# Optimization experiments

Hardware: AMD Instinct MI355X
Metric: run time of the kernel (lower is better)

Reference implementation:

```python
import jax, jax.numpy as jnp
import numpy as np
import math

INPUT_SIZE = 2048
HIDDEN_SIZE = 2048
BATCH = 4096


def setup_inputs() -> dict:
    key = jax.random.key(0)
    ks = jax.random.split(key, 16)
    stdv = 1.0 / math.sqrt(HIDDEN_SIZE)

    def u(k, shape):
        return jax.random.uniform(k, shape, jnp.float32, -stdv, stdv)

    inp = {
        "x": jax.random.normal(ks[0], (BATCH, INPUT_SIZE), jnp.float32),
        "h_x": jax.random.normal(ks[1], (BATCH, HIDDEN_SIZE), jnp.float32),
        "c_x": jax.random.normal(ks[2], (BATCH, HIDDEN_SIZE), jnp.float32),
        "W_xi": u(ks[3], (INPUT_SIZE, HIDDEN_SIZE)),
        "W_hi": u(ks[4], (HIDDEN_SIZE, HIDDEN_SIZE)),
        "b_i": u(ks[5], (HIDDEN_SIZE,)),
        "W_xf": u(ks[6], (INPUT_SIZE, HIDDEN_SIZE)),
        "W_hf": u(ks[7], (HIDDEN_SIZE, HIDDEN_SIZE)),
        "b_f": u(ks[8], (HIDDEN_SIZE,)),
        "W_xc": u(ks[9], (INPUT_SIZE, HIDDEN_SIZE)),
        "W_hc": u(ks[10], (HIDDEN_SIZE, HIDDEN_SIZE)),
        "b_c": u(ks[11], (HIDDEN_SIZE,)),
        "W_xo": u(ks[12], (INPUT_SIZE, HIDDEN_SIZE)),
        "W_ho": u(ks[13], (HIDDEN_SIZE, HIDDEN_SIZE)),
        "b_o": u(ks[14], (HIDDEN_SIZE,)),
    }
    return inp


def reference(x, h_x, c_x, W_xi, W_hi, b_i, W_xf, W_hf, b_f, W_xc, W_hc, b_c, W_xo, W_ho, b_o):
    # LSTM cell: 4 gates, each x @ W_x* + h @ W_h* + b_*
    input_gate = jax.nn.sigmoid(x @ W_xi + h_x @ W_hi + b_i)
    forget_gate = jax.nn.sigmoid(x @ W_xf + h_x @ W_hf + b_f)
    output_gate = jax.nn.sigmoid(x @ W_xo + h_x @ W_ho + b_o)
    c_tilda = jnp.tanh(x @ W_xc + h_x @ W_hc + b_c)
    cy = forget_gate * c_x + input_gate * c_tilda
    hy = output_gate * jnp.tanh(cy)
    return (hy, cy)
```

## Files before the change

### kernel.cpp

```cpp
#include <hip/hip_runtime.h>
#include <stdint.h>

typedef __attribute__((ext_vector_type(8))) short short8;
typedef __attribute__((ext_vector_type(8))) unsigned short ushort8;
typedef __attribute__((ext_vector_type(4))) float floatx4;

#define BATCH 4096
#define HID   2048
#define KTOT  4096

__device__ __forceinline__ uint16_t f2bf(float f) {
    union { uint32_t i; float f; } v; v.f = f;
    uint32_t u = v.i;
    u += 0x7fffu + ((u >> 16) & 1u);
    return (uint16_t)(u >> 16);
}
__device__ __forceinline__ float sigmoid_f(float v) {
    return 1.0f / (1.0f + __expf(-v));
}
__device__ __forceinline__ float tanh_f(float v) {
    v = fminf(fmaxf(v, -15.0f), 15.0f);
    float e = __expf(-2.0f * v);
    return (1.0f - e) / (1.0f + e);
}
__device__ __forceinline__ void load_lds16(const uint16_t* g, uint16_t* l) {
    __builtin_amdgcn_global_load_lds(
        (const __attribute__((address_space(1))) void*)g,
        (__attribute__((address_space(3))) void*)l, 16, 0, 0);
}

__global__ __launch_bounds__(256) void conv_w(
    const float* __restrict__ w0, const float* __restrict__ w1,
    const float* __restrict__ w2, const float* __restrict__ w3,
    const float* __restrict__ w4, const float* __restrict__ w5,
    const float* __restrict__ w6, const float* __restrict__ w7,
    uint16_t* __restrict__ wt)
{
    int b   = blockIdx.x;
    int mi  = b >> 8;
    int rem = b & 255;
    int k0  = (rem >> 4) * 128;
    int n0  = (rem & 15) * 128;
    const float* src;
    switch (mi) {
        case 0: src = w0; break; case 1: src = w1; break;
        case 2: src = w2; break; case 3: src = w3; break;
        case 4: src = w4; break; case 5: src = w5; break;
        case 6: src = w6; break; default: src = w7; break;
    }
    int g = mi >> 1, half = mi & 1;
    int ty = threadIdx.x >> 4, tx = threadIdx.x & 15;
    int kr = k0 + ty * 8;
    int nc = n0 + tx * 8;

    ushort8 a[8];
    #pragma unroll
    for (int j = 0; j < 8; ++j) {
        const float* s = src + (size_t)(kr + j) * HID + nc;
        floatx4 f0 = *(const floatx4*)(s);
        floatx4 f1 = *(const floatx4*)(s + 4);
        #pragma unroll
        for (int i = 0; i < 4; ++i) {
            a[j][i]     = f2bf(f0[i]);
            a[j][4 + i] = f2bf(f1[i]);
        }
    }
    ushort8 bt[8];
    #pragma unroll
    for (int i = 0; i < 8; ++i)
        #pragma unroll
        for (int j = 0; j < 8; ++j)
            bt[i][j] = a[j][i];
    #pragma unroll
    for (int i = 0; i < 8; ++i)
        *(ushort8*)(wt + ((size_t)g * HID + nc + i) * KTOT + half * HID + kr) = bt[i];
}

__global__ __launch_bounds__(256) void conv_a(
    const float* __restrict__ x, const float* __restrict__ h,
    uint16_t* __restrict__ xh)
{
    size_t base = ((size_t)blockIdx.x * 256 + threadIdx.x) * 8;
    int m = (int)(base >> 12);
    int k = (int)(base & (KTOT - 1));
    const float* s = (k < HID) ? (x + (size_t)m * HID + k)
                               : (h + (size_t)m * HID + (k - HID));
    floatx4 f0 = *(const floatx4*)(s);
    floatx4 f1 = *(const floatx4*)(s + 4);
    ushort8 v;
    #pragma unroll
    for (int j = 0; j < 4; ++j) { v[j] = f2bf(f0[j]); v[4 + j] = f2bf(f1[j]); }
    *(ushort8*)(xh + base) = v;
}


#define MFMA16(B0_)                                                           \
    __builtin_amdgcn_s_setprio(1);                                            \
    _Pragma("unroll") for (int i_ = 0; i_ < 4; ++i_)                          \
      _Pragma("unroll") for (int g_ = 0; g_ < 4; ++g_)                        \
        acc[(B0_) + i_][g_] = __builtin_amdgcn_mfma_f32_16x16x32_bf16(        \
            af[i_], bf[g_], acc[(B0_) + i_][g_], 0, 0, 0);                    \
    __builtin_amdgcn_s_setprio(0);

#define DO_TILE(RA, RB, SA, SB, K0S, DOSTAGE)                                 \
  {                                                                           \
               \
    _Pragma("unroll") for (int g_ = 0; g_ < 4; ++g_)                          \
      bf[g_] = *(const short8*)((RB) + g_ * 4096 + pc0e);                     \
    _Pragma("unroll") for (int i_ = 0; i_ < 4; ++i_)                          \
      af[i_] = *(const short8*)((RA) + i_ * 1024 + pc0e);                     \
    if (DOSTAGE) {                                                            \
      _Pragma("unroll") for (int p_ = 0; p_ < 4; ++p_)                        \
        load_lds16(gA + (size_t)p_ * (64 * KTOT) + (K0S), (SA) + p_ * 4096);  \
      _Pragma("unroll") for (int p_ = 0; p_ < 4; ++p_)                        \
        load_lds16(gB + (size_t)p_ * ((size_t)HID * KTOT) + (K0S),            \
                   (SB) + p_ * 4096);                                         \
    }                                                                         \
    __builtin_amdgcn_s_barrier();                                             \
    MFMA16(0)                                                                 \
    __builtin_amdgcn_s_barrier();                                             \
                           \
    _Pragma("unroll") for (int i_ = 0; i_ < 4; ++i_)                          \
      af[i_] = *(const short8*)((RA) + (4 + i_) * 1024 + pc0e);               \
    __builtin_amdgcn_s_barrier();                                             \
    MFMA16(4)                                                                 \
    __builtin_amdgcn_s_barrier();                                             \
                                                 \
    _Pragma("unroll") for (int g_ = 0; g_ < 4; ++g_)                          \
      bf[g_] = *(const short8*)((RB) + g_ * 4096 + pc1e);                     \
    _Pragma("unroll") for (int i_ = 0; i_ < 4; ++i_)                          \
      af[i_] = *(const short8*)((RA) + i_ * 1024 + pc1e);                     \
    __builtin_amdgcn_s_barrier();                                             \
    MFMA16(0)                                                                 \
    __builtin_amdgcn_s_barrier();                                             \
           \
    _Pragma("unroll") for (int i_ = 0; i_ < 4; ++i_)                          \
      af[i_] = *(const short8*)((RA) + (4 + i_) * 1024 + pc1e);               \
    __builtin_amdgcn_s_barrier();                                             \
    MFMA16(4)                                                                 \
    asm volatile("s_waitcnt vmcnt(0)" ::: "memory");                          \
    __builtin_amdgcn_s_barrier();                                             \
  }

__global__ __launch_bounds__(512, 2) void lstm_gemm_bf16(
    const uint16_t* __restrict__ xh, const float* __restrict__ cx,
    const uint16_t* __restrict__ wt,
    const float* __restrict__ bvi, const float* __restrict__ bvf,
    const float* __restrict__ bvo, const float* __restrict__ bvc,
    float* __restrict__ out)
{
    __shared__ uint16_t lds[65536];

    int t = threadIdx.x;

    int linear = blockIdx.x;
    int wg = (linear & 7) * 64 + (linear >> 3);
    int my = wg >> 5;
    int nx = wg & 31;
    int m0 = my * 256;
    int n0 = nx * 64;

    int wave = t >> 6, lane = t & 63;
    int wr = wave >> 2, wc = wave & 3;
    int lrow = lane & 15, quad = lane >> 4;
    int swz  = lrow & 7;

    int srow = t >> 3;
    int schk = (t & 7) ^ (srow & 7);
    const uint16_t* gA = xh + (size_t)(m0 + srow) * KTOT + (size_t)schk * 8;
    const uint16_t* gB = wt + (size_t)(n0 + srow) * KTOT + (size_t)schk * 8;
    uint16_t* sA0 = lds + t * 8;
    uint16_t* sB0 = lds + 16384 + t * 8;
    uint16_t* sA1 = lds + 32768 + t * 8;
    uint16_t* sB1 = lds + 49152 + t * 8;

    int aRow = wr * 128 + lrow;
    int bRow = wc * 16 + lrow;
    int pc0e = (quad ^ swz) * 8;
    int pc1e = ((quad + 4) ^ swz) * 8;
    const uint16_t* rA0 = lds + aRow * 64;
    const uint16_t* rB0 = lds + 16384 + bRow * 64;
    const uint16_t* rA1 = lds + 32768 + aRow * 64;
    const uint16_t* rB1 = lds + 49152 + bRow * 64;

    floatx4 acc[8][4] = {};
    short8 af[4], bf[4];

    #pragma unroll
    for (int p = 0; p < 4; ++p)
        load_lds16(gA + (size_t)p * (64 * KTOT), sA0 + p * 4096);
    #pragma unroll
    for (int p = 0; p < 4; ++p)
        load_lds16(gB + (size_t)p * ((size_t)HID * KTOT), sB0 + p * 4096);
    asm volatile("s_waitcnt vmcnt(0)" ::: "memory");
    __builtin_amdgcn_s_barrier();

    for (int it = 0; it < 32; ++it) {
        size_t k0o = (size_t)it * 128 + 64;
        DO_TILE(rA0, rB0, sA1, sB1, k0o, true);
        DO_TILE(rA1, rB1, sA0, sB0, k0o + 64, it < 31);
    }

    int col = n0 + wc * 16 + lrow;
    float Bi = bvi[col], Bf = bvf[col], Bo = bvo[col], Bc = bvc[col];
    int rowb = m0 + wr * 128 + quad * 4;

    #pragma unroll
    for (int mi = 0; mi < 8; ++mi) {
        #pragma unroll
        for (int r = 0; r < 4; ++r) {
            int row = rowb + mi * 16 + r;
            size_t off = (size_t)row * HID + col;
            float gi = sigmoid_f(acc[mi][0][r] + Bi);
            float gf = sigmoid_f(acc[mi][1][r] + Bf);
            float go = sigmoid_f(acc[mi][2][r] + Bo);
            float gc = tanh_f   (acc[mi][3][r] + Bc);
            float cyv = gf * cx[off] + gi * gc;
            float hyv = go * tanh_f(cyv);
            out[off] = hyv;
            out[(size_t)BATCH * HID + off] = cyv;
        }
    }
}

__global__ __launch_bounds__(256) void lstm_fused_f32(
    const float* __restrict__ x, const float* __restrict__ h,
    const float* __restrict__ cx,
    const float* __restrict__ wxi, const float* __restrict__ whi,
    const float* __restrict__ wxf, const float* __restrict__ whf,
    const float* __restrict__ wxo, const float* __restrict__ who,
    const float* __restrict__ wxc, const float* __restrict__ whc,
    const float* __restrict__ bvi, const float* __restrict__ bvf,
    const float* __restrict__ bvo, const float* __restrict__ bvc,
    float* __restrict__ out)
{
    __shared__ uint16_t ldsA[128 * 32];
    __shared__ uint16_t ldsB[128 * 32];
    uint32_t* ldsB32 = (uint32_t*)ldsB;

    int t    = threadIdx.x;
    int n0   = blockIdx.x * 32;
    int m0   = blockIdx.y * 128;
    int wave = t >> 6, lane = t & 63;
    int wr = wave >> 1, wc = wave & 1;
    int lrow = lane & 15, quad = lane >> 4;
    int srow = t >> 2;
    int sseg = (t & 3) * 8;
    int gw = wave;
    int ng = lane & 3;
    int ka = lane >> 2;
    const float *wxg, *whg;
    switch (gw) {
        case 0:  wxg = wxi; whg = whi; break;
        case 1:  wxg = wxf; whg = whf; break;
        case 2:  wxg = wxo; whg = who; break;
        default: wxg = wxc; whg = whc; break;
    }

    floatx4 acc[4][4] = {};

    for (int kt = 0; kt < KTOT / 32; ++kt) {
        int k0  = kt * 32;
        int k0h = k0 & (HID - 1);
        bool xhalf = (k0 < HID);

        ushort8 va[2];
        uint32_t bw[8];
        const float* a = xhalf ? x : h;
        #pragma unroll
        for (int p = 0; p < 2; ++p) {
            const float* s = a + (size_t)(m0 + srow + p * 64) * HID + k0h + sseg;
            floatx4 f0 = *(const floatx4*)(s);
            floatx4 f1 = *(const floatx4*)(s + 4);
            #pragma unroll
            for (int j = 0; j < 4; ++j) {
                va[p][j]     = (short)f2bf(f0[j]);
                va[p][4 + j] = (short)f2bf(f1[j]);
            }
        }
        const float* wp  = xhalf ? wxg : whg;
        const float* r0p = wp + (size_t)(k0h + 2 * ka) * HID + n0 + ng * 8;
        floatx4 a0 = *(const floatx4*)(r0p);
        floatx4 a1 = *(const floatx4*)(r0p + 4);
        floatx4 b0 = *(const floatx4*)(r0p + HID);
        floatx4 b1 = *(const floatx4*)(r0p + HID + 4);
        #pragma unroll
        for (int j = 0; j < 4; ++j) {
            bw[j]     = (uint32_t)f2bf(a0[j]) | ((uint32_t)f2bf(b0[j]) << 16);
            bw[4 + j] = (uint32_t)f2bf(a1[j]) | ((uint32_t)f2bf(b1[j]) << 16);
        }

        __syncthreads();
        #pragma unroll
        for (int p = 0; p < 2; ++p)
            *(ushort8*)(ldsA + (srow + p * 64) * 32 + sseg) = va[p];
        #pragma unroll
        for (int j = 0; j < 8; ++j)
            ldsB32[(gw * 32 + ng * 8 + j) * 16 + ka] = bw[j];
        __syncthreads();

        short8 af[4], bfr[4];
        #pragma unroll
        for (int mi = 0; mi < 4; ++mi)
            af[mi] = *(const short8*)(ldsA + (wr * 64 + mi * 16 + lrow) * 32 + quad * 8);
        #pragma unroll
        for (int g = 0; g < 4; ++g)
            bfr[g] = *(const short8*)(ldsB + (g * 32 + wc * 16 + lrow) * 32 + quad * 8);

        #pragma unroll
        for (int mi = 0; mi < 4; ++mi)
            #pragma unroll
            for (int g = 0; g < 4; ++g)
                acc[mi][g] = __builtin_amdgcn_mfma_f32_16x16x32_bf16(
                    af[mi], bfr[g], acc[mi][g], 0, 0, 0);
    }

    int col = n0 + wc * 16 + lrow;
    float Bi = bvi[col], Bf = bvf[col], Bo = bvo[col], Bc = bvc[col];
    int rowb = m0 + wr * 64 + quad * 4;

    #pragma unroll
    for (int mi = 0; mi < 4; ++mi) {
        #pragma unroll
        for (int r = 0; r < 4; ++r) {
            int row = rowb + mi * 16 + r;
            size_t off = (size_t)row * HID + col;
            float gi = sigmoid_f(acc[mi][0][r] + Bi);
            float gf = sigmoid_f(acc[mi][1][r] + Bf);
            float go = sigmoid_f(acc[mi][2][r] + Bo);
            float gc = tanh_f   (acc[mi][3][r] + Bc);
            float cyv = gf * cx[off] + gi * gc;
            float hyv = go * tanh_f(cyv);
            out[off] = hyv;
            out[(size_t)BATCH * HID + off] = cyv;
        }
    }
}

extern "C" void kernel_launch(void* const* d_in, const int* in_sizes, int n_in,
                              void* d_out, int out_size, void* d_ws, size_t ws_size,
                              hipStream_t stream) {
    const float* x    = (const float*)d_in[0];
    const float* h_x  = (const float*)d_in[1];
    const float* c_x  = (const float*)d_in[2];
    const float* W_xi = (const float*)d_in[3];
    const float* W_hi = (const float*)d_in[4];
    const float* b_i  = (const float*)d_in[5];
    const float* W_xf = (const float*)d_in[6];
    const float* W_hf = (const float*)d_in[7];
    const float* b_f  = (const float*)d_in[8];
    const float* W_xc = (const float*)d_in[9];
    const float* W_hc = (const float*)d_in[10];
    const float* b_c  = (const float*)d_in[11];
    const float* W_xo = (const float*)d_in[12];
    const float* W_ho = (const float*)d_in[13];
    const float* b_o  = (const float*)d_in[14];

    const size_t WT_BYTES = (size_t)4 * HID * KTOT * sizeof(uint16_t);
    const size_t XH_BYTES = (size_t)BATCH * KTOT * sizeof(uint16_t);

    if (ws_size >= WT_BYTES + XH_BYTES) {
        uint16_t* wt = (uint16_t*)d_ws;
        uint16_t* xh = (uint16_t*)((char*)d_ws + WT_BYTES);
        hipLaunchKernelGGL(conv_w, dim3(8 * 256), dim3(256), 0, stream,
                           W_xi, W_hi, W_xf, W_hf, W_xo, W_ho, W_xc, W_hc, wt);
        hipLaunchKernelGGL(conv_a, dim3((BATCH * KTOT) / (256 * 8)), dim3(256), 0, stream,
                           x, h_x, xh);
        hipLaunchKernelGGL(lstm_gemm_bf16, dim3((BATCH / 256) * (HID / 64)), dim3(512), 0, stream,
                           xh, c_x, wt, b_i, b_f, b_o, b_c, (float*)d_out);
    } else {
        hipLaunchKernelGGL(lstm_fused_f32, dim3(HID / 32, BATCH / 128), dim3(256), 0, stream,
                           x, h_x, c_x,
                           W_xi, W_hi, W_xf, W_hf, W_xo, W_ho, W_xc, W_hc,
                           b_i, b_f, b_o, b_c, (float*)d_out);
    }
}
```

Baseline: 508.0 us.

## Stagger A/B tile prefetch, remap block grid per XCD, coalesce weight transpose via LDS

The main GEMM loop now issues the next A tile early in each stage and the B tile late, then waits with vmcnt(4) instead of draining all loads. This keeps one B tile in flight across the barrier so global-load latency overlaps with MFMA work. Blocks are also remapped so each XCD gets a contiguous 8x8 patch of output tiles, which should improve L2 reuse of A and B. The weight conversion kernel now transposes through a swizzled LDS tile so its global writes are coalesced rows. The trade-off is more complex buffer accounting, where a wrong wait count would cause a data race.

```diff
diff --git a/kernel.cpp b/kernel.cpp
--- a/kernel.cpp
+++ b/kernel.cpp
@@ -36,6 +36,8 @@
     const float* __restrict__ w6, const float* __restrict__ w7,
     uint16_t* __restrict__ wt)
 {
+    __shared__ uint16_t tile[128 * 128];
+
     int b   = blockIdx.x;
     int mi  = b >> 8;
     int rem = b & 255;
@@ -71,9 +73,22 @@
         #pragma unroll
         for (int j = 0; j < 8; ++j)
             bt[i][j] = a[j][i];
+
     #pragma unroll
     for (int i = 0; i < 8; ++i)
-        *(ushort8*)(wt + ((size_t)g * HID + nc + i) * KTOT + half * HID + kr) = bt[i];
+        *(ushort8*)(tile + (tx * 8 + i) * 128 + ((ty ^ tx) & 15) * 8) = bt[i];
+    __syncthreads();
+
+    int t = threadIdx.x;
+    #pragma unroll
+    for (int p = 0; p < 8; ++p) {
+        int r    = p * 16 + (t >> 4);
+        int lc   = t & 15;
+        int phys = lc ^ ((r >> 3) & 15);
+        ushort8 v = *(const ushort8*)(tile + r * 128 + phys * 8);
+        *(ushort8*)(wt + ((size_t)g * HID + n0 + r) * KTOT
+                       + half * HID + k0 + lc * 8) = v;
+    }
 }
 
 __global__ __launch_bounds__(256) void conv_a(
@@ -102,19 +117,20 @@
             af[i_], bf[g_], acc[(B0_) + i_][g_], 0, 0, 0);                    \
     __builtin_amdgcn_s_setprio(0);
 
-#define DO_TILE(RA, RB, SA, SB, K0S, DOSTAGE)                                 \
+#define VM_WAIT4 asm volatile("s_waitcnt vmcnt(4)" ::: "memory")
+#define VM_WAIT0 asm volatile("s_waitcnt vmcnt(0)" ::: "memory")
+#define VM_NONE  ((void)0)
+
+#define DO_TILE(RA, RB, SAN, SBC, KA, KB, DOA, DOB, VMOP)                     \
   {                                                                           \
-               \
+             \
     _Pragma("unroll") for (int g_ = 0; g_ < 4; ++g_)                          \
       bf[g_] = *(const short8*)((RB) + g_ * 4096 + pc0e);                     \
     _Pragma("unroll") for (int i_ = 0; i_ < 4; ++i_)                          \
       af[i_] = *(const short8*)((RA) + i_ * 1024 + pc0e);                     \
-    if (DOSTAGE) {                                                            \
+    if (DOA) {                                                                \
       _Pragma("unroll") for (int p_ = 0; p_ < 4; ++p_)                        \
-        load_lds16(gA + (size_t)p_ * (64 * KTOT) + (K0S), (SA) + p_ * 4096);  \
-      _Pragma("unroll") for (int p_ = 0; p_ < 4; ++p_)                        \
-        load_lds16(gB + (size_t)p_ * ((size_t)HID * KTOT) + (K0S),            \
-                   (SB) + p_ * 4096);                                         \
+        load_lds16(gA + (size_t)p_ * (64 * KTOT) + (KA), (SAN) + p_ * 4096);  \
     }                                                                         \
     __builtin_amdgcn_s_barrier();                                             \
     MFMA16(0)                                                                 \
@@ -125,7 +141,7 @@
     __builtin_amdgcn_s_barrier();                                             \
     MFMA16(4)                                                                 \
     __builtin_amdgcn_s_barrier();                                             \
-                                                 \
+                   \
     _Pragma("unroll") for (int g_ = 0; g_ < 4; ++g_)                          \
       bf[g_] = *(const short8*)((RB) + g_ * 4096 + pc1e);                     \
     _Pragma("unroll") for (int i_ = 0; i_ < 4; ++i_)                          \
@@ -133,12 +149,17 @@
     __builtin_amdgcn_s_barrier();                                             \
     MFMA16(0)                                                                 \
     __builtin_amdgcn_s_barrier();                                             \
-           \
+       \
     _Pragma("unroll") for (int i_ = 0; i_ < 4; ++i_)                          \
       af[i_] = *(const short8*)((RA) + (4 + i_) * 1024 + pc1e);               \
+    if (DOB) {                                                                \
+      _Pragma("unroll") for (int p_ = 0; p_ < 4; ++p_)                        \
+        load_lds16(gB + (size_t)p_ * ((size_t)HID * KTOT) + (KB),             \
+                   (SBC) + p_ * 4096);                                        \
+    }                                                                         \
     __builtin_amdgcn_s_barrier();                                             \
     MFMA16(4)                                                                 \
-    asm volatile("s_waitcnt vmcnt(0)" ::: "memory");                          \
+    VMOP;                                                                     \
     __builtin_amdgcn_s_barrier();                                             \
   }
 
@@ -154,9 +175,10 @@
     int t = threadIdx.x;
 
     int linear = blockIdx.x;
-    int wg = (linear & 7) * 64 + (linear >> 3);
-    int my = wg >> 5;
-    int nx = wg & 31;
+    int xcd = linear & 7;
+    int idx = linear >> 3;
+    int my  = (xcd >> 2) * 8 + (idx >> 3);
+    int nx  = (xcd & 3) * 8 + (idx & 7);
     int m0 = my * 256;
     int n0 = nx * 64;
 
@@ -192,14 +214,19 @@
     #pragma unroll
     for (int p = 0; p < 4; ++p)
         load_lds16(gB + (size_t)p * ((size_t)HID * KTOT), sB0 + p * 4096);
-    asm volatile("s_waitcnt vmcnt(0)" ::: "memory");
+    #pragma unroll
+    for (int p = 0; p < 4; ++p)
+        load_lds16(gB + (size_t)p * ((size_t)HID * KTOT) + 64, sB1 + p * 4096);
+    VM_WAIT4;
     __builtin_amdgcn_s_barrier();
 
-    for (int it = 0; it < 32; ++it) {
-        size_t k0o = (size_t)it * 128 + 64;
-        DO_TILE(rA0, rB0, sA1, sB1, k0o, true);
-        DO_TILE(rA1, rB1, sA0, sB0, k0o + 64, it < 31);
-    }
+    for (int it = 0; it < 31; ++it) {
+        size_t kk = (size_t)it * 128;
+        DO_TILE(rA0, rB0, sA1, sB0, kk + 64,  kk + 128, 1, 1, VM_WAIT4);
+        DO_TILE(rA1, rB1, sA0, sB1, kk + 128, kk + 192, 1, 1, VM_WAIT4);
+    }
+    DO_TILE(rA0, rB0, sA1, sB0, (size_t)63 * 64, 0, 1, 0, VM_WAIT0);
+    DO_TILE(rA1, rB1, sA0, sB1, 0, 0, 0, 0, VM_NONE);
 
     int col = n0 + wc * 16 + lrow;
     float Bi = bvi[col], Bf = bvf[col], Bo = bvo[col], Bc = bvc[col];
```

After: 476.5 us. 1.07x faster.
